# Optimization experiments

Measured on AMD Instinct MI355X. Metric: run time of the kernel, lower is better.

The kernel has to match this reference:

```python
import jax, jax.numpy as jnp
import numpy as np

B, T, C, H = 4, 2048, 768, 768  # batch, seq, embed_size, embed_size_h


def setup_inputs() -> dict:
    key = jax.random.key(0)
    ks = jax.random.split(key, 7)
    s = 1.0 / np.sqrt(C)  # torch Linear default-ish init scale
    return {
        "x": jax.random.normal(ks[0], (B, T, C), jnp.float32),
        "Wq": jax.random.normal(ks[1], (C, H), jnp.float32) * s,
        "bq": jnp.zeros((H,), jnp.float32),
        "Wk": jax.random.normal(ks[2], (C, H), jnp.float32) * s,
        "bk": jnp.zeros((H,), jnp.float32),
        "Wv": jax.random.normal(ks[3], (C, H), jnp.float32) * s,
        "bv": jnp.zeros((H,), jnp.float32),
    }


def reference(x, Wq, bq, Wk, bk, Wv, bv):
    # q,k,v: [B,T,H]
    q = x @ Wq + bq
    k = x @ Wk + bk
    v = x @ Wv + bv
    scale = jnp.asarray(H, x.dtype) ** -0.5
    # full [B,T,T] score matrix, as the original module does
    qk = jnp.einsum("btd,bsd->bts", q, k) * scale
    tril = jnp.tril(jnp.ones((T, T), x.dtype))
    qk = qk * tril
    # original quirk: masked_fill on exact zeros (covers upper triangle)
    qk = jnp.where(qk == 0, -jnp.inf, qk)
    attn = jax.nn.softmax(qk, axis=-1)  # [B,T,T]
    # note: in the source, dropout is applied to a dead value; output uses softmax directly
    return attn @ v  # [B,T,H]
```

## Files before the change

### kernel.cpp

```cpp
#include <hip/hip_runtime.h>
#include <math.h>


#define BB 4
#define TT 2048
#define CC 768

typedef __bf16 bf16_t;
typedef __bf16 bf16x8 __attribute__((ext_vector_type(8)));
typedef _Float16 half8 __attribute__((ext_vector_type(8)));
typedef float f32x4 __attribute__((ext_vector_type(4)));

__device__ __forceinline__ void async_load16(void* lds, const void* g) {
  __builtin_amdgcn_global_load_lds(
      (const __attribute__((address_space(1))) void*)g,
      (__attribute__((address_space(3))) void*)lds, 16, 0, 0);
}

__device__ __forceinline__ int swz4(int r) {
  return (r & 3) ^ ((r >> 2) & 3);
}

__device__ __forceinline__ void stage_tile(const bf16_t* __restrict__ g0,
                                           int ld, bf16_t* lds, int t) {
  int w = t >> 6, l = t & 63;
#pragma unroll
  for (int i = 0; i < 2; ++i) {
    int c = i * 256 + w * 64 + l;
    int row = c >> 2;
    int p = c & 3;
    int q = p ^ swz4(row);
    async_load16(lds + i * 2048 + w * 512,
                 g0 + row * ld + q * 8);
  }
}

__device__ __forceinline__ bf16x8 read_frag(const bf16_t* lds, int r, int q) {
  int p = q ^ swz4(r);
  return *(const bf16x8*)(lds + r * 32 + p * 8);
}

__device__ __forceinline__ void mfma_tile(const bf16_t* Ab, const bf16_t* Bb,
                                          int wr, int wc, int l,
                                          f32x4 acc[4][4]) {
  bf16x8 af[4], bfr[4];
  int q = l >> 4;
#pragma unroll
  for (int i = 0; i < 4; ++i) {
    af[i] = read_frag(Ab, wr + i * 16 + (l & 15), q);
    bfr[i] = read_frag(Bb, wc + i * 16 + (l & 15), q);
  }
#pragma unroll
  for (int mi = 0; mi < 4; ++mi)
#pragma unroll
    for (int ni = 0; ni < 4; ++ni)
      acc[mi][ni] = __builtin_amdgcn_mfma_f32_16x16x32_bf16(
          af[mi], bfr[ni], acc[mi][ni], 0, 0, 0);
}

__device__ __forceinline__ void gemm_core(const bf16_t* __restrict__ A, int lda,
                                          const bf16_t* __restrict__ B, int ldb,
                                          int kTiles, bf16_t* As0, bf16_t* As1,
                                          bf16_t* Bs0, bf16_t* Bs1,
                                          f32x4 acc[4][4]) {
  int t = threadIdx.x;
  int l = t & 63;
  int w = t >> 6;
  int wr = (w >> 1) * 64;
  int wc = (w & 1) * 64;

  stage_tile(A, lda, As0, t);
  stage_tile(B, ldb, Bs0, t);

  for (int kt = 0; kt < kTiles; kt += 2) {
    __syncthreads();
    stage_tile(A + (kt + 1) * 32, lda, As1, t);
    stage_tile(B + (kt + 1) * 32, ldb, Bs1, t);
    mfma_tile(As0, Bs0, wr, wc, l, acc);
    __syncthreads();
    if (kt + 2 < kTiles) {
      stage_tile(A + (kt + 2) * 32, lda, As0, t);
      stage_tile(B + (kt + 2) * 32, ldb, Bs0, t);
    }
    mfma_tile(As1, Bs1, wr, wc, l, acc);
  }
}


__global__ __launch_bounds__(256) void prep_kernel(
    const float* __restrict__ x, const float* __restrict__ Wq,
    const float* __restrict__ Wk, const float* __restrict__ Wv,
    bf16_t* __restrict__ xbf, bf16_t* __restrict__ wt) {
  __shared__ float tile[32][33];
  int bid = blockIdx.x;
  int t = threadIdx.x;
  if (bid < 3072) {
    int i = bid * 256 + t;
    const float4* xin = (const float4*)x;
    float4 a = xin[i * 2];
    float4 b = xin[i * 2 + 1];
    bf16_t tmp[8];
    tmp[0] = (bf16_t)a.x; tmp[1] = (bf16_t)a.y;
    tmp[2] = (bf16_t)a.z; tmp[3] = (bf16_t)a.w;
    tmp[4] = (bf16_t)b.x; tmp[5] = (bf16_t)b.y;
    tmp[6] = (bf16_t)b.z; tmp[7] = (bf16_t)b.w;
    *(uint4*)(xbf + (size_t)i * 8) = *(const uint4*)tmp;
  } else {
    int r = bid - 3072;
    int z = r / 576;
    r -= z * 576;
    int by = r / 24, bx = r - by * 24;
    const float* W = (z == 0) ? Wq : (z == 1) ? Wk : Wv;
    bf16_t* out = wt + (size_t)z * CC * CC;
    int tx = t & 31, ty = t >> 5;
    int n0 = bx * 32, c0 = by * 32;
#pragma unroll
    for (int k = 0; k < 4; ++k)
      tile[ty + k * 8][tx] = W[(size_t)(c0 + ty + k * 8) * CC + n0 + tx];
    __syncthreads();
#pragma unroll
    for (int k = 0; k < 4; ++k)
      out[(size_t)(n0 + ty + k * 8) * CC + c0 + tx] =
          (bf16_t)tile[tx][ty + k * 8];
  }
}

__global__ __launch_bounds__(256) void qkv_gemm_kernel(
    const bf16_t* __restrict__ xbf, const bf16_t* __restrict__ wt,
    const float* __restrict__ bq, const float* __restrict__ bk,
    const float* __restrict__ bv, bf16_t* __restrict__ qb,
    bf16_t* __restrict__ kb, bf16_t* __restrict__ vt) {
  __shared__ bf16_t smem[16384];
  int bid = blockIdx.x;
  int work = (bid & 7) * 144 + (bid >> 3);
  int z = work / 384;
  int rw = work - z * 384;
  int m0 = (rw / 6) * 128;
  int n0 = (rw % 6) * 128;

  f32x4 acc[4][4];
#pragma unroll
  for (int i = 0; i < 4; ++i)
#pragma unroll
    for (int j = 0; j < 4; ++j) acc[i][j] = (f32x4){0.f, 0.f, 0.f, 0.f};

  const bf16_t* A = xbf + (size_t)m0 * CC;
  const bf16_t* B = wt + (size_t)z * CC * CC + (size_t)n0 * CC;
  gemm_core(A, CC, B, CC, CC / 32, smem, smem + 4096, smem + 8192,
            smem + 12288, acc);

  int t = threadIdx.x;
  int l = t & 63, w = t >> 6;
  int wr = (w >> 1) * 64, wc = (w & 1) * 64;
  const float* bias = (z == 0) ? bq : (z == 1) ? bk : bv;

  if (z < 2) {
    float scale = (z == 0) ? rsqrtf((float)CC) : 1.0f;
    bf16_t* dst = (z == 0) ? qb : kb;
#pragma unroll
    for (int mi = 0; mi < 4; ++mi) {
#pragma unroll
      for (int ni = 0; ni < 4; ++ni) {
        int col = n0 + wc + ni * 16 + (l & 15);
        int rbase = m0 + wr + mi * 16 + (l >> 4) * 4;
        float bcol = bias[col];
#pragma unroll
        for (int r = 0; r < 4; ++r) {
          float v = (acc[mi][ni][r] + bcol) * scale;
          dst[(size_t)(rbase + r) * CC + col] = (bf16_t)v;
        }
      }
    }
  } else {
    __syncthreads();
#pragma unroll
    for (int mi = 0; mi < 4; ++mi) {
#pragma unroll
      for (int ni = 0; ni < 4; ++ni) {
        int cl = wc + ni * 16 + (l & 15);
        int mlb = wr + mi * 16 + (l >> 4) * 4;
        float bcol = bias[n0 + cl];
        bf16_t t4[4];
#pragma unroll
        for (int r = 0; r < 4; ++r) t4[r] = (bf16_t)(acc[mi][ni][r] + bcol);
        int e = cl * 128 + (((mlb >> 3) ^ (cl & 15)) << 3) + (mlb & 7);
        *(uint2*)((unsigned int*)smem + (e >> 1)) = *(const uint2*)t4;
      }
    }
    __syncthreads();
    int b = m0 >> 11;
    int tt0 = m0 & (TT - 1);
#pragma unroll
    for (int g = 0; g < 8; ++g) {
      int cl = g * 16 + (t >> 4);
      int ck = t & 15;
      int phys = ck ^ (cl & 15);
      uint4 v = *(const uint4*)(smem + cl * 128 + phys * 8);
      *(uint4*)(vt + ((size_t)b * CC + n0 + cl) * TT + tt0 + ck * 8) = v;
    }
  }
}

__global__ __launch_bounds__(256, 4) void s_gemm_kernel(
    const bf16_t* __restrict__ qb, const bf16_t* __restrict__ kb,
    _Float16* __restrict__ S) {
  __shared__ bf16_t smem[16384];
  int bid = blockIdx.x;
  int work = (bid & 7) * 68 + (bid >> 3);
  int b = work / 136;
  int t = work - b * 136;
  int ti = (int)((sqrtf(8.f * (float)t + 1.f) - 1.f) * 0.5f);
  while ((ti + 1) * (ti + 2) / 2 <= t) ++ti;
  while (ti * (ti + 1) / 2 > t) --ti;
  int tj = t - ti * (ti + 1) / 2;
  int m0 = ti * 128, n0 = tj * 128;

  f32x4 acc[4][4];
#pragma unroll
  for (int i = 0; i < 4; ++i)
#pragma unroll
    for (int j = 0; j < 4; ++j) acc[i][j] = (f32x4){0.f, 0.f, 0.f, 0.f};

  const bf16_t* A = qb + ((size_t)b * TT + m0) * CC;
  const bf16_t* B = kb + ((size_t)b * TT + n0) * CC;
  gemm_core(A, CC, B, CC, CC / 32, smem, smem + 4096, smem + 8192,
            smem + 12288, acc);

  _Float16* Sb = S + (size_t)b * TT * TT;
  _Float16* lds = (_Float16*)smem;
  int tid = threadIdx.x;
  int l = tid & 63, w = tid >> 6;
  int wr = (w >> 1) * 64, wc = (w & 1) * 64;
  __syncthreads();
#pragma unroll
  for (int mi = 0; mi < 4; ++mi) {
#pragma unroll
    for (int ni = 0; ni < 4; ++ni) {
      int cl = wc + ni * 16 + (l & 15);
      int rb = wr + mi * 16 + (l >> 4) * 4;
      int j = n0 + cl;
#pragma unroll
      for (int r = 0; r < 4; ++r) {
        int row = rb + r;
        int i = m0 + row;
        float v = acc[mi][ni][r];
        if (j > i || v == 0.0f) v = -INFINITY;
        lds[row * 128 + (((cl >> 3) ^ (row & 7)) << 3) + (cl & 7)] =
            (_Float16)v;
      }
    }
  }
  __syncthreads();
#pragma unroll
  for (int g = 0; g < 8; ++g) {
    int row = g * 16 + (tid >> 4);
    int ck = tid & 15;
    uint4 v = *(const uint4*)(lds + row * 128 + ((ck ^ (row & 7)) << 3));
    *(uint4*)(Sb + (size_t)(m0 + row) * TT + n0 + ck * 8) = v;
  }
}

__global__ __launch_bounds__(256) void rowstat_kernel(
    const _Float16* __restrict__ S, bf16_t* __restrict__ P) {
  int g = blockIdx.x * 4 + (threadIdx.x >> 6);
  int b = g >> 11;
  int row = g & (TT - 1);
  int l = threadIdx.x & 63;
  const _Float16* s = S + ((size_t)b * TT + row) * TT;
  bf16_t* p = P + ((size_t)b * TT + row) * TT;
  int pe = ((row >> 7) + 1) << 7;

  float f[4][8];
#pragma unroll
  for (int c = 0; c < 4; ++c) {
    int j = (c * 64 + l) * 8;
    if (j < pe) {
      half8 h = *(const half8*)(s + j);
#pragma unroll
      for (int k = 0; k < 8; ++k) f[c][k] = (float)h[k];
    } else {
#pragma unroll
      for (int k = 0; k < 8; ++k) f[c][k] = -INFINITY;
    }
  }

  float m = f[0][0];
#pragma unroll
  for (int c = 0; c < 4; ++c)
#pragma unroll
    for (int k = 0; k < 8; ++k) m = fmaxf(m, f[c][k]);
#pragma unroll
  for (int off = 32; off > 0; off >>= 1) m = fmaxf(m, __shfl_xor(m, off));

  float e[4][8];
  float sum = 0.f;
#pragma unroll
  for (int c = 0; c < 4; ++c)
#pragma unroll
    for (int k = 0; k < 8; ++k) {
      e[c][k] = __expf(f[c][k] - m);
      sum += e[c][k];
    }
#pragma unroll
  for (int off = 32; off > 0; off >>= 1) sum += __shfl_xor(sum, off);
  float inv = 1.0f / sum;

#pragma unroll
  for (int c = 0; c < 4; ++c) {
    int j = (c * 64 + l) * 8;
    if (j < pe) {
      bf16x8 o;
#pragma unroll
      for (int k = 0; k < 8; ++k) o[k] = (bf16_t)(e[c][k] * inv);
      *(bf16x8*)(p + j) = o;
    }
  }
}

__global__ __launch_bounds__(256, 4) void o_gemm_kernel(
    const bf16_t* __restrict__ P, const bf16_t* __restrict__ vt,
    float* __restrict__ out) {
  __shared__ bf16_t smem[16384];
  int bid = blockIdx.x;
  int work = (bid & 7) * 48 + (bid >> 3);
  int b = work / 96;
  int rw = work - b * 96;
  int i = rw / 6, nj = rw % 6;
  int ti = (i & 1) ? ((i - 1) >> 1) : (15 - (i >> 1));
  int m0 = ti * 128, n0 = nj * 128;

  f32x4 acc[4][4];
#pragma unroll
  for (int ii = 0; ii < 4; ++ii)
#pragma unroll
    for (int j = 0; j < 4; ++j) acc[ii][j] = (f32x4){0.f, 0.f, 0.f, 0.f};

  const bf16_t* A = P + ((size_t)b * TT + m0) * TT;
  const bf16_t* B = vt + ((size_t)b * CC + n0) * TT;
  gemm_core(A, TT, B, TT, (ti + 1) * 4, smem, smem + 4096, smem + 8192,
            smem + 12288, acc);

  float* Ob = out + (size_t)b * TT * CC;
  float* lds = (float*)smem;
  int tid = threadIdx.x;
  int l = tid & 63, w = tid >> 6;
  int wr = (w >> 1) * 64, wc = (w & 1) * 64;
  (void)wr;
#pragma unroll
  for (int h = 0; h < 2; ++h) {
    __syncthreads();
    if ((w >> 1) == h) {
#pragma unroll
      for (int mi = 0; mi < 4; ++mi) {
#pragma unroll
        for (int ni = 0; ni < 4; ++ni) {
          int cl = wc + ni * 16 + (l & 15);
          int rb = mi * 16 + (l >> 4) * 4;
#pragma unroll
          for (int r = 0; r < 4; ++r) {
            int row = rb + r;
            lds[row * 128 + ((((cl >> 2) ^ (row & 7)) << 2) | (cl & 3))] =
                acc[mi][ni][r];
          }
        }
      }
    }
    __syncthreads();
#pragma unroll
    for (int g = 0; g < 8; ++g) {
      int row = g * 8 + (tid >> 5);
      int c = tid & 31;
      uint4 v =
          *(const uint4*)(lds + row * 128 + ((c ^ (row & 7)) << 2));
      *(uint4*)(Ob + (size_t)(m0 + h * 64 + row) * CC + n0 + c * 4) = v;
    }
  }
}

extern "C" void kernel_launch(void* const* d_in, const int* in_sizes, int n_in,
                              void* d_out, int out_size, void* d_ws,
                              size_t ws_size, hipStream_t stream) {
  const float* x = (const float*)d_in[0];
  const float* Wq = (const float*)d_in[1];
  const float* bq = (const float*)d_in[2];
  const float* Wk = (const float*)d_in[3];
  const float* bk = (const float*)d_in[4];
  const float* Wv = (const float*)d_in[5];
  const float* bv = (const float*)d_in[6];
  float* out = (float*)d_out;

  char* ws = (char*)d_ws;
  size_t off = 0;
  auto carve = [&](size_t bytes) -> char* {
    char* p = ws + off;
    off += (bytes + 255) & ~(size_t)255;
    return p;
  };
  const size_t M = (size_t)BB * TT;
  bf16_t* xbf = (bf16_t*)carve(M * CC * 2);
  bf16_t* wt  = (bf16_t*)carve(3ull * CC * CC * 2);
  bf16_t* qb  = (bf16_t*)carve(M * CC * 2);
  bf16_t* kb  = (bf16_t*)carve(M * CC * 2);
  bf16_t* vt  = (bf16_t*)carve(M * CC * 2);
  _Float16* S = (_Float16*)carve((size_t)BB * TT * TT * 2);
  bf16_t* P   = (bf16_t*)carve((size_t)BB * TT * TT * 2);
  (void)off; (void)ws_size;

  prep_kernel<<<4800, 256, 0, stream>>>(x, Wq, Wk, Wv, xbf, wt);
  qkv_gemm_kernel<<<1152, 256, 0, stream>>>(xbf, wt, bq, bk, bv, qb, kb, vt);
  s_gemm_kernel<<<544, 256, 0, stream>>>(qb, kb, S);
  rowstat_kernel<<<BB * TT / 4, 256, 0, stream>>>(S, P);
  o_gemm_kernel<<<384, 256, 0, stream>>>(P, vt, out);
}
```

Before: 199.1 us.

## Fuse softmax stats into S GEMM epilogue and normalize on the fly in O GEMM

```diff
diff --git a/kernel.cpp b/kernel.cpp
--- a/kernel.cpp
+++ b/kernel.cpp
@@ -84,6 +84,56 @@
     }
     mfma_tile(As1, Bs1, wr, wc, l, acc);
   }
+}
+
+__device__ __forceinline__ void o_core(const _Float16* __restrict__ Sa,
+                                       const bf16_t* __restrict__ B, int ldb,
+                                       const float2* __restrict__ Mi,
+                                       int kTiles, bf16_t* As0, bf16_t* As1,
+                                       bf16_t* Bs0, bf16_t* Bs1,
+                                       f32x4 acc[4][4]) {
+  int t = threadIdx.x;
+  int l = t & 63;
+  int w = t >> 6;
+  int wr = (w >> 1) * 64;
+  int wc = (w & 1) * 64;
+
+  int c0 = t, c1 = 256 + t;
+  int r0 = c0 >> 2, r1 = c1 >> 2;
+  int q0 = (c0 & 3) ^ swz4(r0), q1 = (c1 & 3) ^ swz4(r1);
+  const _Float16* s0 = Sa + (size_t)r0 * TT + q0 * 8;
+  const _Float16* s1 = Sa + (size_t)r1 * TT + q1 * 8;
+  float2 mi0 = Mi[r0], mi1 = Mi[r1];
+
+#define STAGE_A(dst, kt_)                                        \
+  {                                                              \
+    half8 h0 = *(const half8*)(s0 + (kt_)*32);                   \
+    half8 h1 = *(const half8*)(s1 + (kt_)*32);                   \
+    bf16x8 o0, o1;                                               \
+    _Pragma("unroll") for (int k = 0; k < 8; ++k) {              \
+      o0[k] = (bf16_t)(__expf((float)h0[k] - mi0.x) * mi0.y);    \
+      o1[k] = (bf16_t)(__expf((float)h1[k] - mi1.x) * mi1.y);    \
+    }                                                            \
+    *(bf16x8*)((dst) + c0 * 8) = o0;                             \
+    *(bf16x8*)((dst) + c1 * 8) = o1;                             \
+  }
+
+  STAGE_A(As0, 0)
+  stage_tile(B, ldb, Bs0, t);
+
+  for (int kt = 0; kt < kTiles; kt += 2) {
+    __syncthreads();
+    STAGE_A(As1, kt + 1)
+    stage_tile(B + (kt + 1) * 32, ldb, Bs1, t);
+    mfma_tile(As0, Bs0, wr, wc, l, acc);
+    __syncthreads();
+    if (kt + 2 < kTiles) {
+      STAGE_A(As0, kt + 2)
+      stage_tile(B + (kt + 2) * 32, ldb, Bs0, t);
+    }
+    mfma_tile(As1, Bs1, wr, wc, l, acc);
+  }
+#undef STAGE_A
 }
 
 
@@ -203,7 +253,7 @@
 
 __global__ __launch_bounds__(256, 4) void s_gemm_kernel(
     const bf16_t* __restrict__ qb, const bf16_t* __restrict__ kb,
-    _Float16* __restrict__ S) {
+    _Float16* __restrict__ S, float2* __restrict__ stats) {
   __shared__ bf16_t smem[16384];
   int bid = blockIdx.x;
   int work = (bid & 7) * 68 + (bid >> 3);
@@ -251,75 +301,58 @@
     }
   }
   __syncthreads();
+  float2* st = stats + ((size_t)b * TT + m0) * 17 + tj;
 #pragma unroll
   for (int g = 0; g < 8; ++g) {
     int row = g * 16 + (tid >> 4);
     int ck = tid & 15;
     uint4 v = *(const uint4*)(lds + row * 128 + ((ck ^ (row & 7)) << 3));
     *(uint4*)(Sb + (size_t)(m0 + row) * TT + n0 + ck * 8) = v;
-  }
-}
-
-__global__ __launch_bounds__(256) void rowstat_kernel(
-    const _Float16* __restrict__ S, bf16_t* __restrict__ P) {
-  int g = blockIdx.x * 4 + (threadIdx.x >> 6);
-  int b = g >> 11;
+    const _Float16* hv = (const _Float16*)&v;
+    float m = (float)hv[0];
+#pragma unroll
+    for (int k = 1; k < 8; ++k) m = fmaxf(m, (float)hv[k]);
+    float ls = 0.f;
+    if (m > -INFINITY) {
+#pragma unroll
+      for (int k = 0; k < 8; ++k) ls += __expf((float)hv[k] - m);
+    }
+#pragma unroll
+    for (int off = 1; off < 16; off <<= 1) {
+      float mo = __shfl_xor(m, off);
+      float lo = __shfl_xor(ls, off);
+      float mn = fmaxf(m, mo);
+      float ea = (m == mn) ? 1.f : __expf(m - mn);
+      float eb = (mo == mn) ? 1.f : __expf(mo - mn);
+      ls = ls * ea + lo * eb;
+      m = mn;
+    }
+    if (ck == 0) st[(size_t)row * 17] = make_float2(m, ls);
+  }
+}
+
+__global__ __launch_bounds__(256) void finalize_kernel(
+    const float2* __restrict__ stats, float2* __restrict__ Mi) {
+  int g = blockIdx.x * 256 + threadIdx.x;
   int row = g & (TT - 1);
-  int l = threadIdx.x & 63;
-  const _Float16* s = S + ((size_t)b * TT + row) * TT;
-  bf16_t* p = P + ((size_t)b * TT + row) * TT;
-  int pe = ((row >> 7) + 1) << 7;
-
-  float f[4][8];
-#pragma unroll
-  for (int c = 0; c < 4; ++c) {
-    int j = (c * 64 + l) * 8;
-    if (j < pe) {
-      half8 h = *(const half8*)(s + j);
-#pragma unroll
-      for (int k = 0; k < 8; ++k) f[c][k] = (float)h[k];
-    } else {
-#pragma unroll
-      for (int k = 0; k < 8; ++k) f[c][k] = -INFINITY;
-    }
-  }
-
-  float m = f[0][0];
-#pragma unroll
-  for (int c = 0; c < 4; ++c)
-#pragma unroll
-    for (int k = 0; k < 8; ++k) m = fmaxf(m, f[c][k]);
-#pragma unroll
-  for (int off = 32; off > 0; off >>= 1) m = fmaxf(m, __shfl_xor(m, off));
-
-  float e[4][8];
-  float sum = 0.f;
-#pragma unroll
-  for (int c = 0; c < 4; ++c)
-#pragma unroll
-    for (int k = 0; k < 8; ++k) {
-      e[c][k] = __expf(f[c][k] - m);
-      sum += e[c][k];
-    }
-#pragma unroll
-  for (int off = 32; off > 0; off >>= 1) sum += __shfl_xor(sum, off);
-  float inv = 1.0f / sum;
-
-#pragma unroll
-  for (int c = 0; c < 4; ++c) {
-    int j = (c * 64 + l) * 8;
-    if (j < pe) {
-      bf16x8 o;
-#pragma unroll
-      for (int k = 0; k < 8; ++k) o[k] = (bf16_t)(e[c][k] * inv);
-      *(bf16x8*)(p + j) = o;
-    }
-  }
+  int nt = (row >> 7) + 1;
+  const float2* st = stats + (size_t)g * 17;
+  float2 s0 = st[0];
+  float M = s0.x, L = s0.y;
+  for (int j = 1; j < nt; ++j) {
+    float2 s = st[j];
+    float mn = fmaxf(M, s.x);
+    float ea = (M == mn) ? 1.f : __expf(M - mn);
+    float eb = (s.x == mn) ? 1.f : __expf(s.x - mn);
+    L = L * ea + s.y * eb;
+    M = mn;
+  }
+  Mi[g] = make_float2(M, 1.0f / L);
 }
 
 __global__ __launch_bounds__(256, 4) void o_gemm_kernel(
-    const bf16_t* __restrict__ P, const bf16_t* __restrict__ vt,
-    float* __restrict__ out) {
+    const _Float16* __restrict__ S, const float2* __restrict__ Mi,
+    const bf16_t* __restrict__ vt, float* __restrict__ out) {
   __shared__ bf16_t smem[16384];
   int bid = blockIdx.x;
   int work = (bid & 7) * 48 + (bid >> 3);
@@ -335,17 +368,16 @@
 #pragma unroll
     for (int j = 0; j < 4; ++j) acc[ii][j] = (f32x4){0.f, 0.f, 0.f, 0.f};
 
-  const bf16_t* A = P + ((size_t)b * TT + m0) * TT;
+  const _Float16* A = S + ((size_t)b * TT + m0) * TT;
   const bf16_t* B = vt + ((size_t)b * CC + n0) * TT;
-  gemm_core(A, TT, B, TT, (ti + 1) * 4, smem, smem + 4096, smem + 8192,
-            smem + 12288, acc);
+  o_core(A, B, TT, Mi + (size_t)b * TT + m0, (ti + 1) * 4, smem, smem + 4096,
+         smem + 8192, smem + 12288, acc);
 
   float* Ob = out + (size_t)b * TT * CC;
   float* lds = (float*)smem;
   int tid = threadIdx.x;
   int l = tid & 63, w = tid >> 6;
-  int wr = (w >> 1) * 64, wc = (w & 1) * 64;
-  (void)wr;
+  int wc = (w & 1) * 64;
 #pragma unroll
   for (int h = 0; h < 2; ++h) {
     __syncthreads();
@@ -403,12 +435,13 @@
   bf16_t* kb  = (bf16_t*)carve(M * CC * 2);
   bf16_t* vt  = (bf16_t*)carve(M * CC * 2);
   _Float16* S = (_Float16*)carve((size_t)BB * TT * TT * 2);
-  bf16_t* P   = (bf16_t*)carve((size_t)BB * TT * TT * 2);
+  float2* stats = (float2*)carve(M * 17 * 8);
+  float2* Mi    = (float2*)carve(M * 8);
   (void)off; (void)ws_size;
 
   prep_kernel<<<4800, 256, 0, stream>>>(x, Wq, Wk, Wv, xbf, wt);
   qkv_gemm_kernel<<<1152, 256, 0, stream>>>(xbf, wt, bq, bk, bv, qb, kb, vt);
-  s_gemm_kernel<<<544, 256, 0, stream>>>(qb, kb, S);
-  rowstat_kernel<<<BB * TT / 4, 256, 0, stream>>>(S, P);
-  o_gemm_kernel<<<384, 256, 0, stream>>>(P, vt, out);
-}
+  s_gemm_kernel<<<544, 256, 0, stream>>>(qb, kb, S, stats);
+  finalize_kernel<<<32, 256, 0, stream>>>(stats, Mi);
+  o_gemm_kernel<<<384, 256, 0, stream>>>(S, Mi, vt, out);
+}
```

Measured after the change: 228.3 us. 14.7% more time.
